# Optimization experiments

Hardware: AMD Instinct MI355X
Metric: run time of the kernel (lower is better)

## Reference

```python
import jax, jax.numpy as jnp
import numpy as np

B, S, H, NH = 2, 2048, 1024, 16
HD = H // NH  # 64
SCALE = HD ** -0.5


def setup_inputs() -> dict:
    key = jax.random.key(0)
    k1, k2, k3 = jax.random.split(key, 3)
    x = jax.random.normal(k1, (B, S, H), dtype=jnp.float32)
    w_qkv = jax.random.normal(k2, (H, 3 * H), dtype=jnp.float32) * (H ** -0.5)
    b_qkv = jnp.zeros((3 * H,), dtype=jnp.float32)
    w_out = jax.random.normal(k3, (H, H), dtype=jnp.float32) * (H ** -0.5)
    b_out = jnp.zeros((H,), dtype=jnp.float32)
    return {"x": x, "w_qkv": w_qkv, "b_qkv": b_qkv, "w_out": w_out, "b_out": b_out}


def reference(x, w_qkv, b_qkv, w_out, b_out):
    # qkv projection: [B,S,3H] -> split -> [B,NH,S,HD] each
    qkv = x @ w_qkv + b_qkv
    q, k, v = jnp.split(qkv, 3, axis=-1)
    def heads(t):
        return t.reshape(B, S, NH, HD).transpose(0, 2, 1, 3)  # [B,NH,S,HD]
    q, k, v = heads(q), heads(k), heads(v)
    # full (non-causal) softmax attention; chunking in the original is
    # math-equivalent since each query row attends over all keys
    scores = jnp.einsum('bhqd,bhkd->bhqk', q, k) * SCALE
    attn = jax.nn.softmax(scores, axis=-1)
    out = jnp.einsum('bhqk,bhkd->bhqd', attn, v)  # [B,NH,S,HD]
    out = out.transpose(0, 2, 1, 3).reshape(B, S, H)
    # to_out linear (Dropout is identity in eval mode)
    return out @ w_out + b_out
```

## Files before the change

### kernel.cpp

```cpp
#include <hip/hip_runtime.h>
#include <cstdint>

using u16 = unsigned short;
typedef __bf16 bf16x8 __attribute__((ext_vector_type(8)));
typedef __bf16 bf16x4 __attribute__((ext_vector_type(4)));
typedef float f32x4 __attribute__((ext_vector_type(4)));

#define MFMA16(a, b, c) __builtin_amdgcn_mfma_f32_16x16x32_bf16((a), (b), (c), 0, 0, 0)

__device__ __forceinline__ u16 f2bf(float f) {
  union { float f; uint32_t u; } c; c.f = f;
  uint32_t u = c.u;
  u += 0x7fffu + ((u >> 16) & 1u);
  return (u16)(u >> 16);
}

#if __has_builtin(__builtin_amdgcn_global_load_lds)
#define GLOAD_LDS16(g, l)                                                      \
  __builtin_amdgcn_global_load_lds(                                            \
      (__attribute__((address_space(1))) void*)(g),                            \
      (__attribute__((address_space(3))) void*)(l), 16, 0, 0)
#else
#define GLOAD_LDS16(g, l) do { *(uint4*)(l) = *(const uint4*)(g); } while (0)
#endif


__global__ __launch_bounds__(256) void cvt_f32_bf16(const float* __restrict__ in,
                                                    u16* __restrict__ out) {
  int i = (blockIdx.x * 256 + threadIdx.x) * 4;
  float4 v = *(const float4*)&in[i];
  ushort4 p;
  p.x = f2bf(v.x); p.y = f2bf(v.y); p.z = f2bf(v.z); p.w = f2bf(v.w);
  *(ushort4*)&out[i] = p;
}

__global__ __launch_bounds__(256) void transpose_cvt(const float* __restrict__ in,
                                                     u16* __restrict__ out,
                                                     int R, int C) {
  __shared__ float tile[32][33];
  int bx = blockIdx.x * 32;
  int by = blockIdx.y * 32;
  int tx = threadIdx.x, ty = threadIdx.y;
#pragma unroll
  for (int r2 = 0; r2 < 4; ++r2)
    tile[ty + r2 * 8][tx] = in[(size_t)(by + ty + r2 * 8) * C + bx + tx];
  __syncthreads();
#pragma unroll
  for (int r2 = 0; r2 < 4; ++r2) {
    int c = bx + ty + r2 * 8;
    out[(size_t)c * R + by + tx] = f2bf(tile[tx][ty + r2 * 8]);
  }
}

template <int MODE>
__global__ __launch_bounds__(256, 2) void gemm_bt(
    const u16* __restrict__ A, const u16* __restrict__ Bt,
    const float* __restrict__ bias,
    u16* __restrict__ qb, u16* __restrict__ kb, u16* __restrict__ vb,
    float* __restrict__ outf, int M, int N, int K) {
  __shared__ u16 As[128 * 32];
  __shared__ u16 Bs[128 * 32];
  const int tid = threadIdx.x;
  const int m0 = blockIdx.x * 128;
  const int n0 = blockIdx.y * 128;
  const int lane = tid & 63, w = tid >> 6;
  const int quad = lane >> 4, l16 = lane & 15;
  const int wr = w >> 1, wc = w & 1;

  f32x4 acc[4][4] = {};

  const int r0 = tid >> 2, p0 = tid & 3;
  const int r1 = r0 + 64;
  const int c8 = p0 ^ ((r0 >> 1) & 3);
  const u16* ga0 = A + (size_t)(m0 + r0) * K + c8 * 8;
  const u16* ga1 = A + (size_t)(m0 + r1) * K + c8 * 8;
  const u16* gb0 = Bt + (size_t)(n0 + r0) * K + c8 * 8;
  const u16* gb1 = Bt + (size_t)(n0 + r1) * K + c8 * 8;
  u16* la0 = &As[tid * 8];
  u16* la1 = &As[(tid + 256) * 8];
  u16* lb0 = &Bs[tid * 8];
  u16* lb1 = &Bs[(tid + 256) * 8];

  int aoff[4], boff[4];
#pragma unroll
  for (int i = 0; i < 4; ++i) {
    int ra = wr * 64 + i * 16 + l16;
    aoff[i] = (ra * 4 + (quad ^ ((ra >> 1) & 3))) * 8;
    int rb = wc * 64 + i * 16 + l16;
    boff[i] = (rb * 4 + (quad ^ ((rb >> 1) & 3))) * 8;
  }

  const int nIter = K >> 5;
  for (int kt = 0; kt < nIter; ++kt) {
    __syncthreads();
    const int kk = kt << 5;
    GLOAD_LDS16(ga0 + kk, la0);
    GLOAD_LDS16(ga1 + kk, la1);
    GLOAD_LDS16(gb0 + kk, lb0);
    GLOAD_LDS16(gb1 + kk, lb1);
    __syncthreads();
    bf16x8 af[4], bfr[4];
#pragma unroll
    for (int i = 0; i < 4; ++i) af[i] = *(const bf16x8*)&As[aoff[i]];
#pragma unroll
    for (int j = 0; j < 4; ++j) bfr[j] = *(const bf16x8*)&Bs[boff[j]];
#pragma unroll
    for (int i = 0; i < 4; ++i)
#pragma unroll
      for (int j = 0; j < 4; ++j)
        acc[i][j] = MFMA16(af[i], bfr[j], acc[i][j]);
  }

  const int S = 2048, NH = 16;
#pragma unroll
  for (int i = 0; i < 4; ++i) {
    const int mb = m0 + wr * 64 + i * 16 + quad * 4;
#pragma unroll
    for (int j = 0; j < 4; ++j) {
      const int n = n0 + wc * 64 + j * 16 + l16;
      const float bv = bias[n];
      if (MODE == 1) {
#pragma unroll
        for (int r = 0; r < 4; ++r)
          outf[(size_t)(mb + r) * N + n] = acc[i][j][r] + bv;
      } else {
        const int which = n >> 10;
        const int hn = n & 1023;
        const int h = hn >> 6, d = hn & 63;
        const int b = mb >> 11, s = mb & 2047;
        const int bh = b * NH + h;
        if (which == 2) {
          ushort4 pk;
          pk.x = f2bf(acc[i][j][0] + bv);
          pk.y = f2bf(acc[i][j][1] + bv);
          pk.z = f2bf(acc[i][j][2] + bv);
          pk.w = f2bf(acc[i][j][3] + bv);
          *(ushort4*)&vb[((size_t)bh * 64 + d) * S + s] = pk;
        } else {
          const float sc = (which == 0) ? 0.18033688f : 1.0f;
          u16* dst = (which == 0) ? qb : kb;
#pragma unroll
          for (int r = 0; r < 4; ++r)
            dst[((size_t)bh * S + s + r) * 64 + d] = f2bf((acc[i][j][r] + bv) * sc);
        }
      }
    }
  }
}

__global__ __launch_bounds__(256, 2) void attn_fa(
    const u16* __restrict__ qg, const u16* __restrict__ kg,
    const u16* __restrict__ vg, u16* __restrict__ o) {
  const int S = 2048, NH = 16;
  const int h = blockIdx.x, b = blockIdx.y, qblk = blockIdx.z;
  const int bh = b * NH + h;
  const int tid = threadIdx.x, w = tid >> 6, lane = tid & 63;
  const int quad = lane >> 4, l16 = lane & 15;

  __shared__ u16 Ks[2][4096];
  __shared__ u16 Vs[2][4096];
  __shared__ u16 Ps[4][2048];

  const int q0 = qblk * 128 + w * 32;
  const u16* qp = qg + ((size_t)bh * S + q0 + l16) * 64 + quad * 8;
  const bf16x8 qf00 = *(const bf16x8*)qp;
  const bf16x8 qf01 = *(const bf16x8*)(qp + 32);
  const bf16x8 qf10 = *(const bf16x8*)(qp + 1024);
  const bf16x8 qf11 = *(const bf16x8*)(qp + 1024 + 32);

  f32x4 accO0[4] = {}, accO1[4] = {};
  f32x4 accL0 = {}, accL1 = {};

  bf16x8 ones;
#pragma unroll
  for (int i = 0; i < 8; ++i) ones[i] = (__bf16)1.0f;

  const u16* kbase = kg + (size_t)bh * S * 64;
  const u16* vbase = vg + (size_t)bh * 64 * S;

  const int sr0 = tid >> 3, sp0 = tid & 7;
  const int c8s = sp0 ^ (sr0 & 7);
  const u16* kS0 = kbase + (size_t)sr0 * 64 + c8s * 8;
  const u16* kS1 = kbase + (size_t)(sr0 + 32) * 64 + c8s * 8;
  const u16* vS0 = vbase + (size_t)sr0 * S + c8s * 8;
  const u16* vS1 = vbase + (size_t)(sr0 + 32) * S + c8s * 8;

  int koff[4][2];
#pragma unroll
  for (int ct = 0; ct < 4; ++ct) {
    int row = ct * 16 + l16;
    koff[ct][0] = (row * 8 + (quad ^ (row & 7))) * 8;
    koff[ct][1] = (row * 8 + ((quad + 4) ^ (row & 7))) * 8;
  }
  u16* Pw0 = &Ps[w][l16 * 64];
  u16* Pw1 = Pw0 + 1024;
  int pgx[4];
#pragma unroll
  for (int ct = 0; ct < 4; ++ct) pgx[ct] = ((ct * 4 + quad) ^ l16) * 4;
  const int pr0 = ((quad * 2) ^ l16) * 4;

  GLOAD_LDS16(kS0, &Ks[0][tid * 8]);
  GLOAD_LDS16(kS1, &Ks[0][tid * 8 + 2048]);
  GLOAD_LDS16(vS0, &Vs[0][tid * 8]);
  GLOAD_LDS16(vS1, &Vs[0][tid * 8 + 2048]);

  for (int kt = 0; kt < S / 64; ++kt) {
    const int cur = kt & 1;
    __syncthreads();
    if (kt + 1 < S / 64) {
      const int nb = cur ^ 1;
      GLOAD_LDS16(kS0 + (size_t)(kt + 1) * 4096, &Ks[nb][tid * 8]);
      GLOAD_LDS16(kS1 + (size_t)(kt + 1) * 4096, &Ks[nb][tid * 8 + 2048]);
      GLOAD_LDS16(vS0 + (kt + 1) * 64, &Vs[nb][tid * 8]);
      GLOAD_LDS16(vS1 + (kt + 1) * 64, &Vs[nb][tid * 8 + 2048]);
    }
    const u16* Kc = Ks[cur];
    const u16* Vc = Vs[cur];

    bf16x8 kf0[4], kf1[4];
#pragma unroll
    for (int ct = 0; ct < 4; ++ct) {
      kf0[ct] = *(const bf16x8*)&Kc[koff[ct][0]];
      kf1[ct] = *(const bf16x8*)&Kc[koff[ct][1]];
    }
    f32x4 s0[4] = {}, s1[4] = {};
#pragma unroll
    for (int ct = 0; ct < 4; ++ct) {
      s0[ct] = MFMA16(kf0[ct], qf00, s0[ct]);
      s0[ct] = MFMA16(kf1[ct], qf01, s0[ct]);
      s1[ct] = MFMA16(kf0[ct], qf10, s1[ct]);
      s1[ct] = MFMA16(kf1[ct], qf11, s1[ct]);
    }

#pragma unroll
    for (int ct = 0; ct < 4; ++ct)
#pragma unroll
      for (int r = 0; r < 4; ++r) {
        s0[ct][r] = __builtin_amdgcn_exp2f(s0[ct][r]);
        s1[ct][r] = __builtin_amdgcn_exp2f(s1[ct][r]);
      }

#pragma unroll
    for (int ct = 0; ct < 4; ++ct) {
      bf16x4 a = {(__bf16)s0[ct][0], (__bf16)s0[ct][1],
                  (__bf16)s0[ct][2], (__bf16)s0[ct][3]};
      *(bf16x4*)&Pw0[pgx[ct]] = a;
      bf16x4 c = {(__bf16)s1[ct][0], (__bf16)s1[ct][1],
                  (__bf16)s1[ct][2], (__bf16)s1[ct][3]};
      *(bf16x4*)&Pw1[pgx[ct]] = c;
    }

    bf16x4 t0 = *(const bf16x4*)&Pw0[pr0];
    bf16x4 t1 = *(const bf16x4*)&Pw0[pr0 ^ 4];
    bf16x4 t2 = *(const bf16x4*)&Pw0[pr0 ^ 32];
    bf16x4 t3 = *(const bf16x4*)&Pw0[pr0 ^ 36];
    bf16x8 pf00 = __builtin_shufflevector(t0, t1, 0, 1, 2, 3, 4, 5, 6, 7);
    bf16x8 pf01 = __builtin_shufflevector(t2, t3, 0, 1, 2, 3, 4, 5, 6, 7);
    t0 = *(const bf16x4*)&Pw1[pr0];
    t1 = *(const bf16x4*)&Pw1[pr0 ^ 4];
    t2 = *(const bf16x4*)&Pw1[pr0 ^ 32];
    t3 = *(const bf16x4*)&Pw1[pr0 ^ 36];
    bf16x8 pf10 = __builtin_shufflevector(t0, t1, 0, 1, 2, 3, 4, 5, 6, 7);
    bf16x8 pf11 = __builtin_shufflevector(t2, t3, 0, 1, 2, 3, 4, 5, 6, 7);

    accL0 = MFMA16(ones, pf00, accL0);
    accL0 = MFMA16(ones, pf01, accL0);
    accL1 = MFMA16(ones, pf10, accL1);
    accL1 = MFMA16(ones, pf11, accL1);

#pragma unroll
    for (int ct = 0; ct < 4; ++ct) {
      bf16x8 vf0 = *(const bf16x8*)&Vc[koff[ct][0]];
      bf16x8 vf1 = *(const bf16x8*)&Vc[koff[ct][1]];
      accO0[ct] = MFMA16(vf0, pf00, accO0[ct]);
      accO0[ct] = MFMA16(vf1, pf01, accO0[ct]);
      accO1[ct] = MFMA16(vf0, pf10, accO1[ct]);
      accO1[ct] = MFMA16(vf1, pf11, accO1[ct]);
    }
  }

  const float inv0 = 1.f / accL0[0], inv1 = 1.f / accL1[0];

  const int s0r = q0 + l16, s1r = q0 + 16 + l16;
#pragma unroll
  for (int ct = 0; ct < 4; ++ct) {
    ushort4 pk;
    pk.x = f2bf(accO0[ct][0] * inv0);
    pk.y = f2bf(accO0[ct][1] * inv0);
    pk.z = f2bf(accO0[ct][2] * inv0);
    pk.w = f2bf(accO0[ct][3] * inv0);
    *(ushort4*)&o[(size_t)(b * S + s0r) * 1024 + h * 64 + ct * 16 + quad * 4] = pk;
    pk.x = f2bf(accO1[ct][0] * inv1);
    pk.y = f2bf(accO1[ct][1] * inv1);
    pk.z = f2bf(accO1[ct][2] * inv1);
    pk.w = f2bf(accO1[ct][3] * inv1);
    *(ushort4*)&o[(size_t)(b * S + s1r) * 1024 + h * 64 + ct * 16 + quad * 4] = pk;
  }
}


extern "C" void kernel_launch(void* const* d_in, const int* in_sizes, int n_in,
                              void* d_out, int out_size, void* d_ws, size_t ws_size,
                              hipStream_t stream) {
  const float* x = (const float*)d_in[0];
  const float* w_qkv = (const float*)d_in[1];
  const float* b_qkv = (const float*)d_in[2];
  const float* w_out = (const float*)d_in[3];
  const float* b_out = (const float*)d_in[4];
  float* out = (float*)d_out;

  u16* xb = (u16*)d_ws;
  u16* wqT = xb + 4096 * 1024;
  u16* woT = wqT + 3072 * 1024;
  u16* qb = woT + 1024 * 1024;
  u16* kb = qb + 4194304;
  u16* vb = kb + 4194304;
  u16* ao = vb + 4194304;

  cvt_f32_bf16<<<4096, 256, 0, stream>>>(x, xb);
  dim3 tb(32, 8);
  transpose_cvt<<<dim3(3072 / 32, 1024 / 32), tb, 0, stream>>>(w_qkv, wqT, 1024, 3072);
  transpose_cvt<<<dim3(1024 / 32, 1024 / 32), tb, 0, stream>>>(w_out, woT, 1024, 1024);
  gemm_bt<0><<<dim3(32, 24), 256, 0, stream>>>(xb, wqT, b_qkv, qb, kb, vb, nullptr,
                                               4096, 3072, 1024);
  attn_fa<<<dim3(16, 2, 16), 256, 0, stream>>>(qb, kb, vb, ao);
  gemm_bt<1><<<dim3(32, 8), 256, 0, stream>>>(ao, woT, b_out, nullptr, nullptr, nullptr,
                                              out, 4096, 1024, 1024);
}
```

Baseline: 190.4 us.

## Merge prep kernels, add smaller-tile out GEMM, load V directly to registers

The three conversion and transpose kernels are merged into one launch of 8192 blocks, which removes launch overhead. The output projection gets its own kernel with 64-row tiles, doubling the block count to 512 so more CUs are busy. The attention kernel stops staging V through LDS and has each lane load its V fragments straight from global memory every key tile. This frees LDS and removes the V barrier traffic, but the V loads are no longer prefetched a tile ahead and so may add latency.

```diff
diff --git a/kernel.cpp b/kernel.cpp
--- a/kernel.cpp
+++ b/kernel.cpp
@@ -24,40 +24,42 @@
 #define GLOAD_LDS16(g, l) do { *(uint4*)(l) = *(const uint4*)(g); } while (0)
 #endif
 
-
-__global__ __launch_bounds__(256) void cvt_f32_bf16(const float* __restrict__ in,
-                                                    u16* __restrict__ out) {
-  int i = (blockIdx.x * 256 + threadIdx.x) * 4;
-  float4 v = *(const float4*)&in[i];
-  ushort4 p;
-  p.x = f2bf(v.x); p.y = f2bf(v.y); p.z = f2bf(v.z); p.w = f2bf(v.w);
-  *(ushort4*)&out[i] = p;
-}
-
-__global__ __launch_bounds__(256) void transpose_cvt(const float* __restrict__ in,
-                                                     u16* __restrict__ out,
-                                                     int R, int C) {
+__global__ __launch_bounds__(256) void prep(
+    const float* __restrict__ x, const float* __restrict__ w_qkv,
+    const float* __restrict__ w_out, u16* __restrict__ xb,
+    u16* __restrict__ wqT, u16* __restrict__ woT) {
+  const int bid = blockIdx.x, tid = threadIdx.x;
+  if (bid < 4096) {
+    int i = (bid * 256 + tid) * 4;
+    float4 v = *(const float4*)&x[i];
+    ushort4 p;
+    p.x = f2bf(v.x); p.y = f2bf(v.y); p.z = f2bf(v.z); p.w = f2bf(v.w);
+    *(ushort4*)&xb[i] = p;
+    return;
+  }
   __shared__ float tile[32][33];
-  int bx = blockIdx.x * 32;
-  int by = blockIdx.y * 32;
-  int tx = threadIdx.x, ty = threadIdx.y;
+  int t = bid - 4096;
+  const float* in;
+  u16* outp;
+  int C, bx, by;
+  if (t < 3072) { in = w_qkv; outp = wqT; C = 3072; bx = (t % 96) * 32; by = (t / 96) * 32; }
+  else { t -= 3072; in = w_out; outp = woT; C = 1024; bx = (t % 32) * 32; by = (t / 32) * 32; }
+  const int R = 1024;
+  const int tx = tid & 31, ty = tid >> 5;
 #pragma unroll
   for (int r2 = 0; r2 < 4; ++r2)
     tile[ty + r2 * 8][tx] = in[(size_t)(by + ty + r2 * 8) * C + bx + tx];
   __syncthreads();
 #pragma unroll
-  for (int r2 = 0; r2 < 4; ++r2) {
-    int c = bx + ty + r2 * 8;
-    out[(size_t)c * R + by + tx] = f2bf(tile[tx][ty + r2 * 8]);
-  }
-}
-
-template <int MODE>
-__global__ __launch_bounds__(256, 2) void gemm_bt(
+  for (int r2 = 0; r2 < 4; ++r2)
+    outp[(size_t)(bx + ty + r2 * 8) * R + by + tx] = f2bf(tile[tx][ty + r2 * 8]);
+}
+
+__global__ __launch_bounds__(256, 2) void gemm_qkv(
     const u16* __restrict__ A, const u16* __restrict__ Bt,
     const float* __restrict__ bias,
     u16* __restrict__ qb, u16* __restrict__ kb, u16* __restrict__ vb,
-    float* __restrict__ outf, int M, int N, int K) {
+    int M, int N, int K) {
   __shared__ u16 As[128 * 32];
   __shared__ u16 Bs[128 * 32];
   const int tid = threadIdx.x;
@@ -119,31 +121,95 @@
     for (int j = 0; j < 4; ++j) {
       const int n = n0 + wc * 64 + j * 16 + l16;
       const float bv = bias[n];
-      if (MODE == 1) {
+      const int which = n >> 10;
+      const int hn = n & 1023;
+      const int h = hn >> 6, d = hn & 63;
+      const int b = mb >> 11, s = mb & 2047;
+      const int bh = b * NH + h;
+      if (which == 2) {
+        ushort4 pk;
+        pk.x = f2bf(acc[i][j][0] + bv);
+        pk.y = f2bf(acc[i][j][1] + bv);
+        pk.z = f2bf(acc[i][j][2] + bv);
+        pk.w = f2bf(acc[i][j][3] + bv);
+        *(ushort4*)&vb[((size_t)bh * 64 + d) * S + s] = pk;
+      } else {
+        const float sc = (which == 0) ? 0.18033688f : 1.0f;
+        u16* dst = (which == 0) ? qb : kb;
 #pragma unroll
         for (int r = 0; r < 4; ++r)
-          outf[(size_t)(mb + r) * N + n] = acc[i][j][r] + bv;
-      } else {
-        const int which = n >> 10;
-        const int hn = n & 1023;
-        const int h = hn >> 6, d = hn & 63;
-        const int b = mb >> 11, s = mb & 2047;
-        const int bh = b * NH + h;
-        if (which == 2) {
-          ushort4 pk;
-          pk.x = f2bf(acc[i][j][0] + bv);
-          pk.y = f2bf(acc[i][j][1] + bv);
-          pk.z = f2bf(acc[i][j][2] + bv);
-          pk.w = f2bf(acc[i][j][3] + bv);
-          *(ushort4*)&vb[((size_t)bh * 64 + d) * S + s] = pk;
-        } else {
-          const float sc = (which == 0) ? 0.18033688f : 1.0f;
-          u16* dst = (which == 0) ? qb : kb;
-#pragma unroll
-          for (int r = 0; r < 4; ++r)
-            dst[((size_t)bh * S + s + r) * 64 + d] = f2bf((acc[i][j][r] + bv) * sc);
-        }
+          dst[((size_t)bh * S + s + r) * 64 + d] = f2bf((acc[i][j][r] + bv) * sc);
       }
+    }
+  }
+}
+
+__global__ __launch_bounds__(256, 2) void gemm_out(
+    const u16* __restrict__ A, const u16* __restrict__ Bt,
+    const float* __restrict__ bias, float* __restrict__ outf,
+    int M, int N, int K) {
+  __shared__ u16 As[64 * 32];
+  __shared__ u16 Bs[128 * 32];
+  const int tid = threadIdx.x;
+  const int m0 = blockIdx.x * 64;
+  const int n0 = blockIdx.y * 128;
+  const int lane = tid & 63, w = tid >> 6;
+  const int quad = lane >> 4, l16 = lane & 15;
+  const int wr = w >> 1, wc = w & 1;
+
+  f32x4 acc[2][4] = {};
+
+  const int r0 = tid >> 2, p0 = tid & 3;
+  const int c8 = p0 ^ ((r0 >> 1) & 3);
+  const u16* ga0 = A + (size_t)(m0 + r0) * K + c8 * 8;
+  const u16* gb0 = Bt + (size_t)(n0 + r0) * K + c8 * 8;
+  const u16* gb1 = Bt + (size_t)(n0 + r0 + 64) * K + c8 * 8;
+  u16* la0 = &As[tid * 8];
+  u16* lb0 = &Bs[tid * 8];
+  u16* lb1 = &Bs[(tid + 256) * 8];
+
+  int aoff[2], boff[4];
+#pragma unroll
+  for (int i = 0; i < 2; ++i) {
+    int ra = wr * 32 + i * 16 + l16;
+    aoff[i] = (ra * 4 + (quad ^ ((ra >> 1) & 3))) * 8;
+  }
+#pragma unroll
+  for (int j = 0; j < 4; ++j) {
+    int rb = wc * 64 + j * 16 + l16;
+    boff[j] = (rb * 4 + (quad ^ ((rb >> 1) & 3))) * 8;
+  }
+
+  const int nIter = K >> 5;
+  for (int kt = 0; kt < nIter; ++kt) {
+    __syncthreads();
+    const int kk = kt << 5;
+    GLOAD_LDS16(ga0 + kk, la0);
+    GLOAD_LDS16(gb0 + kk, lb0);
+    GLOAD_LDS16(gb1 + kk, lb1);
+    __syncthreads();
+    bf16x8 af[2], bfr[4];
+#pragma unroll
+    for (int i = 0; i < 2; ++i) af[i] = *(const bf16x8*)&As[aoff[i]];
+#pragma unroll
+    for (int j = 0; j < 4; ++j) bfr[j] = *(const bf16x8*)&Bs[boff[j]];
+#pragma unroll
+    for (int i = 0; i < 2; ++i)
+#pragma unroll
+      for (int j = 0; j < 4; ++j)
+        acc[i][j] = MFMA16(af[i], bfr[j], acc[i][j]);
+  }
+
+#pragma unroll
+  for (int i = 0; i < 2; ++i) {
+    const int mb = m0 + wr * 32 + i * 16 + quad * 4;
+#pragma unroll
+    for (int j = 0; j < 4; ++j) {
+      const int n = n0 + wc * 64 + j * 16 + l16;
+      const float bv = bias[n];
+#pragma unroll
+      for (int r = 0; r < 4; ++r)
+        outf[(size_t)(mb + r) * N + n] = acc[i][j][r] + bv;
     }
   }
 }
@@ -158,7 +224,6 @@
   const int quad = lane >> 4, l16 = lane & 15;
 
   __shared__ u16 Ks[2][4096];
-  __shared__ u16 Vs[2][4096];
   __shared__ u16 Ps[4][2048];
 
   const int q0 = qblk * 128 + w * 32;
@@ -182,8 +247,6 @@
   const int c8s = sp0 ^ (sr0 & 7);
   const u16* kS0 = kbase + (size_t)sr0 * 64 + c8s * 8;
   const u16* kS1 = kbase + (size_t)(sr0 + 32) * 64 + c8s * 8;
-  const u16* vS0 = vbase + (size_t)sr0 * S + c8s * 8;
-  const u16* vS1 = vbase + (size_t)(sr0 + 32) * S + c8s * 8;
 
   int koff[4][2];
 #pragma unroll
@@ -192,6 +255,11 @@
     koff[ct][0] = (row * 8 + (quad ^ (row & 7))) * 8;
     koff[ct][1] = (row * 8 + ((quad + 4) ^ (row & 7))) * 8;
   }
+  const u16* vrow[4];
+#pragma unroll
+  for (int ct = 0; ct < 4; ++ct)
+    vrow[ct] = vbase + (size_t)(ct * 16 + l16) * S + quad * 8;
+
   u16* Pw0 = &Ps[w][l16 * 64];
   u16* Pw1 = Pw0 + 1024;
   int pgx[4];
@@ -201,21 +269,24 @@
 
   GLOAD_LDS16(kS0, &Ks[0][tid * 8]);
   GLOAD_LDS16(kS1, &Ks[0][tid * 8 + 2048]);
-  GLOAD_LDS16(vS0, &Vs[0][tid * 8]);
-  GLOAD_LDS16(vS1, &Vs[0][tid * 8 + 2048]);
 
   for (int kt = 0; kt < S / 64; ++kt) {
     const int cur = kt & 1;
     __syncthreads();
+
+    bf16x8 vf0[4], vf1[4];
+#pragma unroll
+    for (int ct = 0; ct < 4; ++ct) {
+      vf0[ct] = *(const bf16x8*)(vrow[ct] + kt * 64);
+      vf1[ct] = *(const bf16x8*)(vrow[ct] + kt * 64 + 32);
+    }
+
     if (kt + 1 < S / 64) {
       const int nb = cur ^ 1;
       GLOAD_LDS16(kS0 + (size_t)(kt + 1) * 4096, &Ks[nb][tid * 8]);
       GLOAD_LDS16(kS1 + (size_t)(kt + 1) * 4096, &Ks[nb][tid * 8 + 2048]);
-      GLOAD_LDS16(vS0 + (kt + 1) * 64, &Vs[nb][tid * 8]);
-      GLOAD_LDS16(vS1 + (kt + 1) * 64, &Vs[nb][tid * 8 + 2048]);
     }
     const u16* Kc = Ks[cur];
-    const u16* Vc = Vs[cur];
 
     bf16x8 kf0[4], kf1[4];
 #pragma unroll
@@ -270,12 +341,10 @@
 
 #pragma unroll
     for (int ct = 0; ct < 4; ++ct) {
-      bf16x8 vf0 = *(const bf16x8*)&Vc[koff[ct][0]];
-      bf16x8 vf1 = *(const bf16x8*)&Vc[koff[ct][1]];
-      accO0[ct] = MFMA16(vf0, pf00, accO0[ct]);
-      accO0[ct] = MFMA16(vf1, pf01, accO0[ct]);
-      accO1[ct] = MFMA16(vf0, pf10, accO1[ct]);
-      accO1[ct] = MFMA16(vf1, pf11, accO1[ct]);
+      accO0[ct] = MFMA16(vf0[ct], pf00, accO0[ct]);
+      accO0[ct] = MFMA16(vf1[ct], pf01, accO0[ct]);
+      accO1[ct] = MFMA16(vf0[ct], pf10, accO1[ct]);
+      accO1[ct] = MFMA16(vf1[ct], pf11, accO1[ct]);
     }
   }
 
@@ -317,13 +386,10 @@
   u16* vb = kb + 4194304;
   u16* ao = vb + 4194304;
 
-  cvt_f32_bf16<<<4096, 256, 0, stream>>>(x, xb);
-  dim3 tb(32, 8);
-  transpose_cvt<<<dim3(3072 / 32, 1024 / 32), tb, 0, stream>>>(w_qkv, wqT, 1024, 3072);
-  transpose_cvt<<<dim3(1024 / 32, 1024 / 32), tb, 0, stream>>>(w_out, woT, 1024, 1024);
-  gemm_bt<0><<<dim3(32, 24), 256, 0, stream>>>(xb, wqT, b_qkv, qb, kb, vb, nullptr,
-                                               4096, 3072, 1024);
+  prep<<<8192, 256, 0, stream>>>(x, w_qkv, w_out, xb, wqT, woT);
+  gemm_qkv<<<dim3(32, 24), 256, 0, stream>>>(xb, wqT, b_qkv, qb, kb, vb,
+                                             4096, 3072, 1024);
   attn_fa<<<dim3(16, 2, 16), 256, 0, stream>>>(qb, kb, vb, ao);
-  gemm_bt<1><<<dim3(32, 8), 256, 0, stream>>>(ao, woT, b_out, nullptr, nullptr, nullptr,
-                                              out, 4096, 1024, 1024);
-}
+  gemm_out<<<dim3(64, 8), 256, 0, stream>>>(ao, woT, b_out, out,
+                                            4096, 1024, 1024);
+}
```

After: 238.6 us. +25.3%, slower.
